# Kernel tuning notes

Measured on AMD Instinct MI355X. Metric: run time of the kernel, lower is better.

Reference implementation:

```python
import jax, jax.numpy as jnp
import numpy as np

N_P = 200000  # points (literals)
N_C = 50000   # constraints (clauses)
D = 64
VOCAB = 400   # max_size**2 = 20**2


def setup_inputs() -> dict:
    key = jax.random.key(0)
    ks = jax.random.split(key, 12)
    s = 0.05
    inp = {}
    inp["embedding"] = jax.random.normal(ks[0], (VOCAB, D)) * s
    inp["cls_bias"] = jnp.zeros((VOCAB,))
    inp["W_cinit"] = jax.random.normal(ks[1], (D, 1)) * s
    inp["b_cinit"] = jnp.zeros((D,))
    # clause LSTMs stacked in c_t order: 0=equi, 1=square, 2=diamond, 3=midpoint
    inp["Wih_c"] = jax.random.normal(ks[2], (4, 4 * D, 4 * D)) * s
    inp["Whh_c"] = jax.random.normal(ks[3], (4, 4 * D, D)) * s
    inp["bih_c"] = jnp.zeros((4, 4 * D))
    inp["bhh_c"] = jnp.zeros((4, 4 * D))
    # point-update LSTM L_u
    inp["Wih_u"] = jax.random.normal(ks[4], (4 * D, D)) * s
    inp["Whh_u"] = jax.random.normal(ks[5], (4 * D, D)) * s
    inp["bih_u"] = jnp.zeros((4 * D,))
    inp["bhh_u"] = jnp.zeros((4 * D,))
    inp["x_p_rand"] = jax.random.uniform(ks[6], (N_P, D))
    inp["y"] = jax.random.randint(ks[7], (N_P,), 0, VOCAB)
    inp["p_t"] = jax.random.randint(ks[8], (N_P,), 0, 2)
    inp["c_t"] = jax.random.randint(ks[9], (N_C,), 0, 4)
    inp["p2c"] = jax.random.randint(ks[10], (N_C, 4), 0, N_P)
    inp["num_iters"] = 2
    return inp


def _lstm_cell(x, h, c, Wih, Whh, bih, bhh):
    # torch nn.LSTM single-step cell, gate order (i, f, g, o)
    gates = x @ Wih.T + bih + h @ Whh.T + bhh
    i, f, g, o = jnp.split(gates, 4, axis=-1)
    c_new = jax.nn.sigmoid(f) * c + jax.nn.sigmoid(i) * jnp.tanh(g)
    h_new = jax.nn.sigmoid(o) * jnp.tanh(c_new)
    return h_new, c_new


def reference(embedding, cls_bias, W_cinit, b_cinit, Wih_c, Whh_c, bih_c, bhh_c,
              Wih_u, Whh_u, bih_u, bhh_u, x_p_rand, y, p_t, c_t, p2c, num_iters):
    n_p, d = x_p_rand.shape
    n_c = c_t.shape[0]
    fixed = (p_t != 0)[:, None]  # fixed points keep their embedding
    x_p = jnp.where(fixed, embedding[y], x_p_rand)
    c_init = W_cinit[:, 0] + b_cinit  # C_init(ones(1))
    x_c = jnp.broadcast_to(c_init, (n_c, d))
    x_p_h = jnp.zeros_like(x_p)
    x_c_h = jnp.zeros_like(x_c)
    sel = jax.nn.one_hot(c_t, 4, dtype=x_p.dtype)  # [n_c, 4] clause-type selector
    flat_p2c = p2c.reshape(-1)
    for _ in range(num_iters):
        # LC: gather the 4 points of each constraint
        vars_ = x_p[p2c]  # [n_c, 4, d]
        vars_full = vars_.reshape(n_c, 4 * d)
        vars_mid = vars_.at[:, 3].set(0.0).reshape(n_c, 4 * d)  # midpoint zeros 4th slot
        hs, cs = [], []
        for tp in range(4):
            inp_t = vars_mid if tp == 3 else vars_full
            h_t, c_new = _lstm_cell(inp_t, x_c, x_c_h, Wih_c[tp], Whh_c[tp], bih_c[tp], bhh_c[tp])
            hs.append(h_t)
            cs.append(c_new)
        hs = jnp.stack(hs)  # [4, n_c, d]
        cs = jnp.stack(cs)
        x_c = jnp.einsum('tnd,nt->nd', hs, sel)
        x_c_h = jnp.einsum('tnd,nt->nd', cs, sel)
        # CL: msg = adj.T @ x_c, i.e. scatter-add x_c over incidence edges
        msg = jax.ops.segment_sum(jnp.repeat(x_c, 4, axis=0), flat_p2c, num_segments=n_p)
        h_u, c_u = _lstm_cell(msg, x_p, x_p_h, Wih_u, Whh_u, bih_u, bhh_u)
        # only variable points are updated; fixed points keep old state
        x_p = jnp.where(fixed, x_p, h_u)
        x_p_h = jnp.where(fixed, x_p_h, c_u)
    logits = x_p @ embedding.T + cls_bias  # tied classifier
    return logits
```

## Files before the change

### kernel.cpp

```cpp
#include <hip/hip_runtime.h>
#include <hip/hip_bf16.h>

#define DD 64
#define GG 256

typedef __attribute__((ext_vector_type(8))) __bf16 bfrag;
typedef __attribute__((ext_vector_type(4))) float f32x4;

__device__ __forceinline__ float sigmf(float x){ return 1.f/(1.f+__expf(-x)); }
__device__ __forceinline__ float tanhfast(float x){ return 1.f - 2.f/(__expf(2.f*x)+1.f); }
__device__ __forceinline__ short bf16c(float f){
  __hip_bfloat16 h = __float2bfloat16(f);
  return *reinterpret_cast<short*>(&h);
}

__global__ void k_setup(
    const float* __restrict__ Wihc, const float* __restrict__ Whhc,
    const float* __restrict__ Wihu, const float* __restrict__ Whhu,
    const float* __restrict__ emb, const float* __restrict__ Wci,
    const float* __restrict__ bci, const float* __restrict__ xpr,
    const int* __restrict__ y, const int* __restrict__ pt,
    const int* __restrict__ ct, const int* __restrict__ p2c,
    short* __restrict__ Wc_lay, short* __restrict__ Wu_lay,
    short* __restrict__ E_lay,
    short* __restrict__ xp_bf, short* __restrict__ xc_bf,
    int* __restrict__ tlist, int* __restrict__ cnt,
    int* __restrict__ vlist, int* __restrict__ cnt2,
    int* __restrict__ deg, int NP, int NC)
{
  int b = blockIdx.x;
  const int t = threadIdx.x;
  if (b < 1280){
    int idx = b*256 + t;
    int tp = idx / 81920, r = idx % 81920;
    int ks = r / 8192;  int r2 = r % 8192;
    int nt = r2 / 512;  int r3 = r2 % 512;
    int lr = r3 / 32;   int r4 = r3 % 32;
    int lk = r4 / 8,    e  = r4 % 8;
    int g = nt*16 + lr, k = ks*32 + lk*8 + e;
    float v = (k < 256) ? Wihc[((size_t)tp*256+g)*256 + k]
                        : Whhc[((size_t)tp*256+g)*64 + (k-256)];
    Wc_lay[idx] = bf16c(v);
    return;
  }
  b -= 1280;
  if (b < 128){
    int idx = b*256 + t;
    int ks = idx / 8192; int r2 = idx % 8192;
    int nt = r2 / 512;   int r3 = r2 % 512;
    int lr = r3 / 32;    int r4 = r3 % 32;
    int lk = r4 / 8,     e  = r4 % 8;
    int g = nt*16 + lr, k = ks*32 + lk*8 + e;
    float v = (k < 64) ? Wihu[g*64 + k] : Whhu[g*64 + (k-64)];
    Wu_lay[idx] = bf16c(v);
    return;
  }
  b -= 128;
  if (b < 100){
    int idx = b*256 + t;
    int ks = idx / 12800; int r = idx % 12800;
    int nt = r / 512;     int r3 = r % 512;
    int lr = r3 / 32;     int r4 = r3 % 32;
    int lk = r4 / 8,      e  = r4 % 8;
    int v = nt*16 + lr, k = ks*32 + lk*8 + e;
    E_lay[idx] = bf16c(emb[v*64 + k]);
    return;
  }
  b -= 100;
  int nbP4 = (NP*4 + 255) >> 8;
  if (b < nbP4){
    int i = b*256 + t;
    if (i < NP*4){
      int p = i >> 2, ch = i & 3;
      const float* src = (pt[p]!=0) ? (emb + (size_t)y[p]*DD + ch*16)
                                    : (xpr + (size_t)p*DD + ch*16);
      short o[16];
      #pragma unroll
      for (int f4=0; f4<4; ++f4){
        float4 v = ((const float4*)src)[f4];
        o[f4*4+0]=bf16c(v.x); o[f4*4+1]=bf16c(v.y); o[f4*4+2]=bf16c(v.z); o[f4*4+3]=bf16c(v.w);
      }
      *(uint4*)(xp_bf + (size_t)p*DD + ch*16)     = *(uint4*)&o[0];
      *(uint4*)(xp_bf + (size_t)p*DD + ch*16 + 8) = *(uint4*)&o[8];
    }
    return;
  }
  b -= nbP4;
  int nbC4 = (NC*4 + 255) >> 8;
  if (b < nbC4){
    int i = b*256 + t;
    if (i < NC*4){
      int c = i >> 2, ch = i & 3;
      short o[16];
      #pragma unroll
      for (int d=0; d<16; ++d) o[d] = bf16c(Wci[ch*16+d] + bci[ch*16+d]);
      *(uint4*)(xc_bf + (size_t)c*DD + ch*16)     = *(uint4*)&o[0];
      *(uint4*)(xc_bf + (size_t)c*DD + ch*16 + 8) = *(uint4*)&o[8];
    }
    return;
  }
  b -= nbC4;
  int nbCl = (NC + 255) >> 8;
  if (b < nbCl){
    int c = b*256 + t;
    int lane = t & 63;
    int tp = (c < NC) ? ct[c] : -1;
    unsigned long long lt = (lane == 63) ? ~0ull >> 1 : ((1ull << lane) - 1ull);
    #pragma unroll
    for (int ty=0; ty<4; ++ty){
      unsigned long long m = __ballot(tp==ty);
      if (m == 0ull) continue;
      int nw = __popcll(m), rank = __popcll(m & lt);
      int leader = __ffsll((long long)m) - 1;
      int base = 0;
      if (lane == leader) base = atomicAdd(cnt + ty, nw);
      base = __shfl(base, leader);
      if (tp == ty) tlist[ty*NC + base + rank] = c;
    }
    return;
  }
  b -= nbCl;
  int nbCp = (NP + 255) >> 8;
  if (b < nbCp){
    int p = b*256 + t;
    int lane = t & 63;
    bool var = (p < NP) && (pt[p]==0);
    unsigned long long lt = (lane == 63) ? ~0ull >> 1 : ((1ull << lane) - 1ull);
    unsigned long long m = __ballot(var);
    if (m){
      int nw = __popcll(m), rank = __popcll(m & lt);
      int leader = __ffsll((long long)m) - 1;
      int base = 0;
      if (lane == leader) base = atomicAdd(cnt2, nw);
      base = __shfl(base, leader);
      if (var) vlist[base + rank] = p;
    }
    return;
  }
  b -= nbCp;
  {
    int e = b*256 + t;
    if (e < NC*4) atomicAdd(deg + p2c[e], 1);
  }
}

__global__ void k_rowstart(const int* __restrict__ deg, int* __restrict__ rowstart,
                           int* __restrict__ gtot, int NP){
  int p = blockIdx.x*256 + threadIdx.x;
  int lane = threadIdx.x & 63;
  int d = (p < NP) ? deg[p] : 0;
  int pre = d;
  #pragma unroll
  for (int off=1; off<64; off<<=1){
    int v = __shfl_up(pre, off);
    if (lane >= off) pre += v;
  }
  int tot = __shfl(pre, 63);
  int base = 0;
  if (lane == 63 && tot) base = atomicAdd(gtot, tot);
  base = __shfl(base, 63);
  if (p < NP) rowstart[p] = base + pre - d;
}
__global__ void k_fill(const int* __restrict__ p2c, const int* __restrict__ rowstart,
                       int* __restrict__ cursor, int* __restrict__ elist, int NE){
  int e = blockIdx.x*256 + threadIdx.x;
  if (e >= NE) return;
  int p = p2c[e];
  int pos = atomicAdd(cursor + p, 1);
  elist[rowstart[p] + pos] = e >> 2;
}

__launch_bounds__(256)
__global__ void k_clause(const short* __restrict__ Wc_lay,
                         const float* __restrict__ bih, const float* __restrict__ bhh,
                         const short* __restrict__ xp_bf,
                         short* __restrict__ xc_bf, float* __restrict__ xch,
                         const int* __restrict__ p2c, const int* __restrict__ tlist,
                         const int* __restrict__ cnt, int NC, int first){
  __shared__ __align__(16) short As[64][328];
  int tp, n, base;
  {
    const int c0=cnt[0], c1=cnt[1], c2=cnt[2], c3=cnt[3];
    int b = blockIdx.x;
    const int t0=(c0+63)>>6;
    if (b < t0){ tp=0; n=c0; base=b<<6; }
    else { b-=t0; const int t1=(c1+63)>>6;
      if (b < t1){ tp=1; n=c1; base=b<<6; }
      else { b-=t1; const int t2=(c2+63)>>6;
        if (b < t2){ tp=2; n=c2; base=b<<6; }
        else { b-=t2; const int t3=(c3+63)>>6;
          if (b < t3){ tp=3; n=c3; base=b<<6; } else return; } } }
  }
  const int t = threadIdx.x;
  {
    int row = t >> 2, ch = t & 3;
    int idx = base + row;
    int c = (idx < n) ? tlist[tp*NC + idx] : -1;
    #pragma unroll
    for (int slot=0; slot<5; ++slot){
      uint4 v0 = make_uint4(0,0,0,0), v1 = make_uint4(0,0,0,0);
      const short* src = nullptr;
      if (c >= 0){
        if (slot < 4){
          if (!(tp==3 && slot==3)){
            int p = p2c[c*4 + slot];
            src = xp_bf + (size_t)p*DD + ch*16;
          }
        } else src = xc_bf + (size_t)c*DD + ch*16;
      }
      if (src){ v0 = *(const uint4*)src; v1 = *(const uint4*)(src+8); }
      *(uint4*)&As[row][slot*64 + ch*16 + 0] = v0;
      *(uint4*)&As[row][slot*64 + ch*16 + 8] = v1;
    }
  }
  __syncthreads();
  const int lane = t & 63, w = t >> 6;
  const int lr = lane & 15, lk = lane >> 4;
  f32x4 acc[16];
  #pragma unroll
  for (int i=0;i<16;i++) acc[i] = (f32x4){0.f,0.f,0.f,0.f};
  const short* wb = Wc_lay + (size_t)tp*81920 + (lr*4 + lk)*8;
  #pragma unroll
  for (int ks=0; ks<10; ++ks){
    bfrag a = *(const bfrag*)&As[w*16 + lr][ks*32 + lk*8];
    #pragma unroll
    for (int nt=0; nt<16; ++nt){
      bfrag bv = *(const bfrag*)(wb + (ks*16 + nt)*512);
      acc[nt] = __builtin_amdgcn_mfma_f32_16x16x32_bf16(a, bv, acc[nt], 0, 0, 0);
    }
  }
  #pragma unroll
  for (int r=0; r<4; ++r){
    int idx = base + w*16 + lk*4 + r;
    if (idx >= n) continue;
    int c = tlist[tp*NC + idx];
    #pragma unroll
    for (int q=0; q<4; ++q){
      int d = lr + 16*q;
      float gi = acc[q][r]    + bih[tp*GG + d]       + bhh[tp*GG + d];
      float gf = acc[4+q][r]  + bih[tp*GG + 64 + d]  + bhh[tp*GG + 64 + d];
      float gn = acc[8+q][r]  + bih[tp*GG + 128 + d] + bhh[tp*GG + 128 + d];
      float go = acc[12+q][r] + bih[tp*GG + 192 + d] + bhh[tp*GG + 192 + d];
      float cold = first ? 0.f : xch[(size_t)c*DD + d];
      float cn = sigmf(gf)*cold + sigmf(gi)*tanhfast(gn);
      float hn = sigmf(go)*tanhfast(cn);
      xc_bf[(size_t)c*DD + d] = bf16c(hn);
      xch[(size_t)c*DD + d]   = cn;
    }
  }
}

__launch_bounds__(256)
__global__ void k_point(const short* __restrict__ Wu_lay,
                        const float* __restrict__ bihu, const float* __restrict__ bhhu,
                        const short* __restrict__ xc_bf,
                        const int* __restrict__ rowstart, const int* __restrict__ deg,
                        const int* __restrict__ elist, const int* __restrict__ vlist,
                        const int* __restrict__ nvp,
                        short* __restrict__ xp_bf, float* __restrict__ xph,
                        int NP, int first){
  const int nv = nvp[0];
  const int base = blockIdx.x*64;
  if (base >= nv) return;
  __shared__ __align__(16) short As[64][136];
  const int t = threadIdx.x;
  {
    int row = t >> 2, ch = t & 3;
    int idx = base + row;
    int gr = (idx < nv) ? vlist[idx] : -1;
    float s[16];
    #pragma unroll
    for (int z=0; z<16; ++z) s[z] = 0.f;
    uint4 xv0 = make_uint4(0,0,0,0), xv1 = make_uint4(0,0,0,0);
    if (gr >= 0){
      int rs = rowstart[gr], dg = deg[gr];
      for (int j=0; j<dg; ++j){
        int c = elist[rs + j];
        const uint4* xcp = (const uint4*)(xc_bf + (size_t)c*DD + ch*16);
        uint4 u0 = xcp[0], u1 = xcp[1];
        uint ua[8] = {u0.x,u0.y,u0.z,u0.w,u1.x,u1.y,u1.z,u1.w};
        #pragma unroll
        for (int i2=0;i2<8;i2++){
          s[i2*2]   += __uint_as_float(ua[i2] << 16);
          s[i2*2+1] += __uint_as_float(ua[i2] & 0xffff0000u);
        }
      }
      const uint4* xpp = (const uint4*)(xp_bf + (size_t)gr*DD + ch*16);
      xv0 = xpp[0]; xv1 = xpp[1];
    }
    short os[16];
    #pragma unroll
    for (int z=0; z<16; ++z) os[z] = bf16c(s[z]);
    *(uint4*)&As[row][ch*16 + 0] = *(uint4*)&os[0];
    *(uint4*)&As[row][ch*16 + 8] = *(uint4*)&os[8];
    *(uint4*)&As[row][64 + ch*16 + 0] = xv0;
    *(uint4*)&As[row][64 + ch*16 + 8] = xv1;
  }
  __syncthreads();
  const int lane = t & 63, w = t >> 6;
  const int lr = lane & 15, lk = lane >> 4;
  f32x4 acc[16];
  #pragma unroll
  for (int i=0;i<16;i++) acc[i] = (f32x4){0.f,0.f,0.f,0.f};
  const short* wb = Wu_lay + (lr*4 + lk)*8;
  #pragma unroll
  for (int ks=0; ks<4; ++ks){
    bfrag a = *(const bfrag*)&As[w*16 + lr][ks*32 + lk*8];
    #pragma unroll
    for (int nt=0; nt<16; ++nt){
      bfrag bv = *(const bfrag*)(wb + (ks*16 + nt)*512);
      acc[nt] = __builtin_amdgcn_mfma_f32_16x16x32_bf16(a, bv, acc[nt], 0, 0, 0);
    }
  }
  #pragma unroll
  for (int r=0; r<4; ++r){
    int idx = base + w*16 + lk*4 + r;
    if (idx >= nv) continue;
    int m = vlist[idx];
    #pragma unroll
    for (int q=0; q<4; ++q){
      int d = lr + 16*q;
      float gi = acc[q][r]    + bihu[d]       + bhhu[d];
      float gf = acc[4+q][r]  + bihu[64 + d]  + bhhu[64 + d];
      float gn = acc[8+q][r]  + bihu[128 + d] + bhhu[128 + d];
      float go = acc[12+q][r] + bihu[192 + d] + bhhu[192 + d];
      float cold = first ? 0.f : xph[(size_t)idx*DD + d];
      float cn = sigmf(gf)*cold + sigmf(gi)*tanhfast(gn);
      float hn = sigmf(go)*tanhfast(cn);
      xp_bf[(size_t)m*DD + d] = bf16c(hn);
      xph[(size_t)idx*DD + d] = cn;
    }
  }
}

__launch_bounds__(256)
__global__ void k_logits(const short* __restrict__ xp_bf, const short* __restrict__ E_lay,
                         const float* __restrict__ cbias,
                         float* __restrict__ out, int NP, int V){
  const int t = threadIdx.x;
  const int lane = t & 63, w = t >> 6;
  const int lr = lane & 15, lk = lane >> 4;
  const int p = blockIdx.x*64 + w*16 + lr;
  const int nt0 = blockIdx.y*5;
  const bool ok = p < NP;
  f32x4 acc[5];
  #pragma unroll
  for (int j=0;j<5;j++) acc[j] = (f32x4){0.f,0.f,0.f,0.f};
  const short* ab = E_lay + (lr*4 + lk)*8;
  #pragma unroll
  for (int ks=0; ks<2; ++ks){
    bfrag b;
    if (ok) b = *(const bfrag*)(xp_bf + (size_t)p*DD + ks*32 + lk*8);
    else    b = (bfrag){0,0,0,0,0,0,0,0};
    #pragma unroll
    for (int j=0; j<5; ++j){
      bfrag a = *(const bfrag*)(ab + (ks*25 + nt0 + j)*512);
      acc[j] = __builtin_amdgcn_mfma_f32_16x16x32_bf16(a, b, acc[j], 0, 0, 0);
    }
  }
  if (!ok) return;
  #pragma unroll
  for (int j=0; j<5; ++j){
    int v = (nt0 + j)*16 + lk*4;
    float4 cb = *(const float4*)(cbias + v);
    float4 r;
    r.x = acc[j][0] + cb.x;
    r.y = acc[j][1] + cb.y;
    r.z = acc[j][2] + cb.z;
    r.w = acc[j][3] + cb.w;
    *(float4*)(out + (size_t)p*V + v) = r;
  }
}

extern "C" void kernel_launch(void* const* d_in, const int* in_sizes, int n_in,
                              void* d_out, int out_size, void* d_ws, size_t ws_size,
                              hipStream_t stream){
  const float* emb   = (const float*)d_in[0];
  const float* cbias = (const float*)d_in[1];
  const float* Wci   = (const float*)d_in[2];
  const float* bci   = (const float*)d_in[3];
  const float* Wihc  = (const float*)d_in[4];
  const float* Whhc  = (const float*)d_in[5];
  const float* bihc  = (const float*)d_in[6];
  const float* bhhc  = (const float*)d_in[7];
  const float* Wihu  = (const float*)d_in[8];
  const float* Whhu  = (const float*)d_in[9];
  const float* bihu  = (const float*)d_in[10];
  const float* bhhu  = (const float*)d_in[11];
  const float* xpr   = (const float*)d_in[12];
  const int* y    = (const int*)d_in[13];
  const int* pt   = (const int*)d_in[14];
  const int* ct   = (const int*)d_in[15];
  const int* p2c  = (const int*)d_in[16];
  const int NP = in_sizes[13];
  const int NC = in_sizes[15];
  const int V  = in_sizes[1];
  const int NE = NC*4;

  char* w = (char*)d_ws;
  auto alloc = [&](size_t bytes)->char*{ char* p = w; w += (bytes + 255) & ~255ull; return p; };
  short* xp_bf = (short*)alloc((size_t)NP*DD*2);
  float* xph   = (float*)alloc((size_t)NP*DD*4);
  short* xc_bf = (short*)alloc((size_t)NC*DD*2);
  float* xch   = (float*)alloc((size_t)NC*DD*4);
  int*   tlist = (int*)alloc((size_t)4*NC*4);
  short* Wc_lay= (short*)alloc((size_t)327680*2);
  short* Wu_lay= (short*)alloc((size_t)32768*2);
  short* E_lay = (short*)alloc((size_t)25600*2);
  int*   deg     = (int*)alloc((size_t)NP*4);
  int*   cursor  = (int*)alloc((size_t)NP*4);
  int*   ctr     = (int*)alloc(256);
  int*   rowstart= (int*)alloc((size_t)NP*4);
  int*   elist   = (int*)alloc((size_t)NE*4);
  int*   vlist   = (int*)alloc((size_t)NP*4);
  int* cnt  = ctr;
  int* cnt2 = ctr + 16;
  int* gtot = ctr + 17;

  const int NB   = (NP + 255)/256;
  const int nbP4 = (NP*4 + 255)/256;
  const int nbC4 = (NC*4 + 255)/256;
  const int nbCl = (NC + 255)/256;
  const int nbCp = NB;
  const int nbE  = (NE + 255)/256;
  const int g_setup = 1280 + 128 + 100 + nbP4 + nbC4 + nbCl + nbCp + nbE;

  hipMemsetAsync(deg, 0, (size_t)NP*8 + 256, stream);
  k_setup<<<g_setup, 256, 0, stream>>>(Wihc, Whhc, Wihu, Whhu, emb, Wci, bci, xpr,
                                       y, pt, ct, p2c,
                                       Wc_lay, Wu_lay, E_lay,
                                       xp_bf, xc_bf,
                                       tlist, cnt, vlist, cnt2, deg, NP, NC);
  k_rowstart<<<NB, 256, 0, stream>>>(deg, rowstart, gtot, NP);
  k_fill<<<nbE, 256, 0, stream>>>(p2c, rowstart, cursor, elist, NE);

  const int ctiles = (NC+63)/64 + 3;
  const int num_iters = 2;
  for (int it=0; it<num_iters; ++it){
    k_clause<<<ctiles, 256, 0, stream>>>(Wc_lay, bihc, bhhc, xp_bf, xc_bf, xch,
                                         p2c, tlist, cnt, NC, it==0);
    k_point<<<(NP+63)/64, 256, 0, stream>>>(Wu_lay, bihu, bhhu, xc_bf,
                                            rowstart, deg, elist, vlist, cnt2,
                                            xp_bf, xph, NP, it==0);
  }
  const int ngv = (V/16 + 4)/5;
  k_logits<<<dim3((NP+63)/64, ngv), 256, 0, stream>>>(xp_bf, E_lay, cbias,
                                                      (float*)d_out, NP, V);
}
```

Before: 456.6 us.

## Fuse all stages into one persistent cooperative kernel with grid syncs

Replaces the memset, setup, rowstart, fill, per-iteration clause/point kernels and logits kernel with a single persistent cooperative kernel. Blocks loop over work items and separate stages with grid-wide syncs. The logits stage is also restructured so each block computes all vocab tiles per point tile in two accumulator batches. This removes multiple kernel launches and launch gaps. In exchange, grid.sync costs are added, occupancy is limited by launch_bounds(256,3) and the shared LDS buffer, and the grid is capped at 2048 blocks.

```diff
diff --git a/kernel.cpp b/kernel.cpp
--- a/kernel.cpp
+++ b/kernel.cpp
@@ -1,5 +1,8 @@
 #include <hip/hip_runtime.h>
 #include <hip/hip_bf16.h>
+#include <hip/hip_cooperative_groups.h>
+
+namespace cg = cooperative_groups;
 
 #define DD 64
 #define GG 256
@@ -14,361 +17,378 @@
   return *reinterpret_cast<short*>(&h);
 }
 
-__global__ void k_setup(
+__launch_bounds__(256, 3)
+__global__ void k_mega(
     const float* __restrict__ Wihc, const float* __restrict__ Whhc,
     const float* __restrict__ Wihu, const float* __restrict__ Whhu,
-    const float* __restrict__ emb, const float* __restrict__ Wci,
-    const float* __restrict__ bci, const float* __restrict__ xpr,
-    const int* __restrict__ y, const int* __restrict__ pt,
+    const float* __restrict__ emb,  const float* __restrict__ Wci,
+    const float* __restrict__ bci,  const float* __restrict__ xpr,
+    const int* __restrict__ y,  const int* __restrict__ pt,
     const int* __restrict__ ct, const int* __restrict__ p2c,
-    short* __restrict__ Wc_lay, short* __restrict__ Wu_lay,
-    short* __restrict__ E_lay,
-    short* __restrict__ xp_bf, short* __restrict__ xc_bf,
-    int* __restrict__ tlist, int* __restrict__ cnt,
-    int* __restrict__ vlist, int* __restrict__ cnt2,
-    int* __restrict__ deg, int NP, int NC)
+    const float* __restrict__ bihc, const float* __restrict__ bhhc,
+    const float* __restrict__ bihu, const float* __restrict__ bhhu,
+    const float* __restrict__ cbias,
+    short* __restrict__ Wc_lay, short* __restrict__ Wu_lay, short* __restrict__ E_lay,
+    short* __restrict__ xp_bf,  short* __restrict__ xc_bf,
+    float* __restrict__ xph,    float* __restrict__ xch,
+    int* __restrict__ tlist, int* __restrict__ vlist,
+    int* __restrict__ deg, int* __restrict__ cursor, int* __restrict__ ctr,
+    int* __restrict__ rowstart, int* __restrict__ elist,
+    float* __restrict__ out, int NP, int NC, int V)
 {
-  int b = blockIdx.x;
+  cg::grid_group grid = cg::this_grid();
+  __shared__ __align__(16) short As[64][328];
   const int t = threadIdx.x;
-  if (b < 1280){
-    int idx = b*256 + t;
-    int tp = idx / 81920, r = idx % 81920;
-    int ks = r / 8192;  int r2 = r % 8192;
-    int nt = r2 / 512;  int r3 = r2 % 512;
-    int lr = r3 / 32;   int r4 = r3 % 32;
-    int lk = r4 / 8,    e  = r4 % 8;
-    int g = nt*16 + lr, k = ks*32 + lk*8 + e;
-    float v = (k < 256) ? Wihc[((size_t)tp*256+g)*256 + k]
-                        : Whhc[((size_t)tp*256+g)*64 + (k-256)];
-    Wc_lay[idx] = bf16c(v);
-    return;
-  }
-  b -= 1280;
-  if (b < 128){
-    int idx = b*256 + t;
-    int ks = idx / 8192; int r2 = idx % 8192;
-    int nt = r2 / 512;   int r3 = r2 % 512;
-    int lr = r3 / 32;    int r4 = r3 % 32;
-    int lk = r4 / 8,     e  = r4 % 8;
-    int g = nt*16 + lr, k = ks*32 + lk*8 + e;
-    float v = (k < 64) ? Wihu[g*64 + k] : Whhu[g*64 + (k-64)];
-    Wu_lay[idx] = bf16c(v);
-    return;
-  }
-  b -= 128;
-  if (b < 100){
-    int idx = b*256 + t;
-    int ks = idx / 12800; int r = idx % 12800;
-    int nt = r / 512;     int r3 = r % 512;
-    int lr = r3 / 32;     int r4 = r3 % 32;
-    int lk = r4 / 8,      e  = r4 % 8;
-    int v = nt*16 + lr, k = ks*32 + lk*8 + e;
-    E_lay[idx] = bf16c(emb[v*64 + k]);
-    return;
-  }
-  b -= 100;
-  int nbP4 = (NP*4 + 255) >> 8;
-  if (b < nbP4){
-    int i = b*256 + t;
-    if (i < NP*4){
-      int p = i >> 2, ch = i & 3;
-      const float* src = (pt[p]!=0) ? (emb + (size_t)y[p]*DD + ch*16)
-                                    : (xpr + (size_t)p*DD + ch*16);
-      short o[16];
-      #pragma unroll
-      for (int f4=0; f4<4; ++f4){
-        float4 v = ((const float4*)src)[f4];
-        o[f4*4+0]=bf16c(v.x); o[f4*4+1]=bf16c(v.y); o[f4*4+2]=bf16c(v.z); o[f4*4+3]=bf16c(v.w);
-      }
-      *(uint4*)(xp_bf + (size_t)p*DD + ch*16)     = *(uint4*)&o[0];
-      *(uint4*)(xp_bf + (size_t)p*DD + ch*16 + 8) = *(uint4*)&o[8];
-    }
-    return;
-  }
-  b -= nbP4;
-  int nbC4 = (NC*4 + 255) >> 8;
-  if (b < nbC4){
-    int i = b*256 + t;
-    if (i < NC*4){
-      int c = i >> 2, ch = i & 3;
-      short o[16];
-      #pragma unroll
-      for (int d=0; d<16; ++d) o[d] = bf16c(Wci[ch*16+d] + bci[ch*16+d]);
-      *(uint4*)(xc_bf + (size_t)c*DD + ch*16)     = *(uint4*)&o[0];
-      *(uint4*)(xc_bf + (size_t)c*DD + ch*16 + 8) = *(uint4*)&o[8];
-    }
-    return;
-  }
-  b -= nbC4;
-  int nbCl = (NC + 255) >> 8;
-  if (b < nbCl){
-    int c = b*256 + t;
-    int lane = t & 63;
-    int tp = (c < NC) ? ct[c] : -1;
-    unsigned long long lt = (lane == 63) ? ~0ull >> 1 : ((1ull << lane) - 1ull);
-    #pragma unroll
-    for (int ty=0; ty<4; ++ty){
-      unsigned long long m = __ballot(tp==ty);
-      if (m == 0ull) continue;
-      int nw = __popcll(m), rank = __popcll(m & lt);
-      int leader = __ffsll((long long)m) - 1;
-      int base = 0;
-      if (lane == leader) base = atomicAdd(cnt + ty, nw);
-      base = __shfl(base, leader);
-      if (tp == ty) tlist[ty*NC + base + rank] = c;
-    }
-    return;
-  }
-  b -= nbCl;
-  int nbCp = (NP + 255) >> 8;
-  if (b < nbCp){
-    int p = b*256 + t;
-    int lane = t & 63;
-    bool var = (p < NP) && (pt[p]==0);
-    unsigned long long lt = (lane == 63) ? ~0ull >> 1 : ((1ull << lane) - 1ull);
-    unsigned long long m = __ballot(var);
-    if (m){
-      int nw = __popcll(m), rank = __popcll(m & lt);
-      int leader = __ffsll((long long)m) - 1;
-      int base = 0;
-      if (lane == leader) base = atomicAdd(cnt2, nw);
-      base = __shfl(base, leader);
-      if (var) vlist[base + rank] = p;
-    }
-    return;
-  }
-  b -= nbCp;
-  {
-    int e = b*256 + t;
-    if (e < NC*4) atomicAdd(deg + p2c[e], 1);
-  }
-}
-
-__global__ void k_rowstart(const int* __restrict__ deg, int* __restrict__ rowstart,
-                           int* __restrict__ gtot, int NP){
-  int p = blockIdx.x*256 + threadIdx.x;
-  int lane = threadIdx.x & 63;
-  int d = (p < NP) ? deg[p] : 0;
-  int pre = d;
-  #pragma unroll
-  for (int off=1; off<64; off<<=1){
-    int v = __shfl_up(pre, off);
-    if (lane >= off) pre += v;
-  }
-  int tot = __shfl(pre, 63);
-  int base = 0;
-  if (lane == 63 && tot) base = atomicAdd(gtot, tot);
-  base = __shfl(base, 63);
-  if (p < NP) rowstart[p] = base + pre - d;
-}
-__global__ void k_fill(const int* __restrict__ p2c, const int* __restrict__ rowstart,
-                       int* __restrict__ cursor, int* __restrict__ elist, int NE){
-  int e = blockIdx.x*256 + threadIdx.x;
-  if (e >= NE) return;
-  int p = p2c[e];
-  int pos = atomicAdd(cursor + p, 1);
-  elist[rowstart[p] + pos] = e >> 2;
-}
-
-__launch_bounds__(256)
-__global__ void k_clause(const short* __restrict__ Wc_lay,
-                         const float* __restrict__ bih, const float* __restrict__ bhh,
-                         const short* __restrict__ xp_bf,
-                         short* __restrict__ xc_bf, float* __restrict__ xch,
-                         const int* __restrict__ p2c, const int* __restrict__ tlist,
-                         const int* __restrict__ cnt, int NC, int first){
-  __shared__ __align__(16) short As[64][328];
-  int tp, n, base;
-  {
-    const int c0=cnt[0], c1=cnt[1], c2=cnt[2], c3=cnt[3];
-    int b = blockIdx.x;
-    const int t0=(c0+63)>>6;
-    if (b < t0){ tp=0; n=c0; base=b<<6; }
-    else { b-=t0; const int t1=(c1+63)>>6;
-      if (b < t1){ tp=1; n=c1; base=b<<6; }
-      else { b-=t1; const int t2=(c2+63)>>6;
-        if (b < t2){ tp=2; n=c2; base=b<<6; }
-        else { b-=t2; const int t3=(c3+63)>>6;
-          if (b < t3){ tp=3; n=c3; base=b<<6; } else return; } } }
-  }
-  const int t = threadIdx.x;
-  {
-    int row = t >> 2, ch = t & 3;
-    int idx = base + row;
-    int c = (idx < n) ? tlist[tp*NC + idx] : -1;
-    #pragma unroll
-    for (int slot=0; slot<5; ++slot){
-      uint4 v0 = make_uint4(0,0,0,0), v1 = make_uint4(0,0,0,0);
-      const short* src = nullptr;
-      if (c >= 0){
-        if (slot < 4){
-          if (!(tp==3 && slot==3)){
-            int p = p2c[c*4 + slot];
-            src = xp_bf + (size_t)p*DD + ch*16;
-          }
-        } else src = xc_bf + (size_t)c*DD + ch*16;
-      }
-      if (src){ v0 = *(const uint4*)src; v1 = *(const uint4*)(src+8); }
-      *(uint4*)&As[row][slot*64 + ch*16 + 0] = v0;
-      *(uint4*)&As[row][slot*64 + ch*16 + 8] = v1;
-    }
-  }
-  __syncthreads();
+  const int nblk = gridDim.x;
   const int lane = t & 63, w = t >> 6;
   const int lr = lane & 15, lk = lane >> 4;
-  f32x4 acc[16];
-  #pragma unroll
-  for (int i=0;i<16;i++) acc[i] = (f32x4){0.f,0.f,0.f,0.f};
-  const short* wb = Wc_lay + (size_t)tp*81920 + (lr*4 + lk)*8;
-  #pragma unroll
-  for (int ks=0; ks<10; ++ks){
-    bfrag a = *(const bfrag*)&As[w*16 + lr][ks*32 + lk*8];
-    #pragma unroll
-    for (int nt=0; nt<16; ++nt){
-      bfrag bv = *(const bfrag*)(wb + (ks*16 + nt)*512);
-      acc[nt] = __builtin_amdgcn_mfma_f32_16x16x32_bf16(a, bv, acc[nt], 0, 0, 0);
+  int* cnt  = ctr;
+  int* cnt2 = ctr + 16;
+  int* gtot = ctr + 17;
+  const int NE = NC*4;
+
+  for (int i = blockIdx.x*256 + t; i < NP; i += nblk*256) deg[i] = 0;
+  for (int i = blockIdx.x*256 + t; i < NP; i += nblk*256) cursor[i] = 0;
+  if (blockIdx.x == 0 && t < 64) ctr[t] = 0;
+  grid.sync();
+
+  {
+    const int nbP4 = (NP*4 + 255) >> 8;
+    const int nbC4 = (NC*4 + 255) >> 8;
+    const int nbCl = (NC + 255) >> 8;
+    const int nbCp = (NP + 255) >> 8;
+    const int nbE  = (NE + 255) >> 8;
+    const int W = 1280 + 128 + 100 + nbP4 + nbC4 + nbCl + nbCp + nbE;
+    for (int wk = blockIdx.x; wk < W; wk += nblk){
+      int b = wk;
+      if (b < 1280){
+        int idx = b*256 + t;
+        int tp = idx / 81920, r = idx % 81920;
+        int ks = r / 8192;  int r2 = r % 8192;
+        int nt = r2 / 512;  int r3 = r2 % 512;
+        int lrr = r3 / 32;  int r4 = r3 % 32;
+        int lkk = r4 / 8,   e  = r4 % 8;
+        int g = nt*16 + lrr, k = ks*32 + lkk*8 + e;
+        float v = (k < 256) ? Wihc[((size_t)tp*256+g)*256 + k]
+                            : Whhc[((size_t)tp*256+g)*64 + (k-256)];
+        Wc_lay[idx] = bf16c(v);
+      } else if ((b -= 1280) < 128){
+        int idx = b*256 + t;
+        int ks = idx / 8192; int r2 = idx % 8192;
+        int nt = r2 / 512;   int r3 = r2 % 512;
+        int lrr = r3 / 32;   int r4 = r3 % 32;
+        int lkk = r4 / 8,    e  = r4 % 8;
+        int g = nt*16 + lrr, k = ks*32 + lkk*8 + e;
+        float v = (k < 64) ? Wihu[g*64 + k] : Whhu[g*64 + (k-64)];
+        Wu_lay[idx] = bf16c(v);
+      } else if ((b -= 128) < 100){
+        int idx = b*256 + t;
+        int ks = idx / 12800; int r = idx % 12800;
+        int nt = r / 512;     int r3 = r % 512;
+        int lrr = r3 / 32;    int r4 = r3 % 32;
+        int lkk = r4 / 8,     e  = r4 % 8;
+        int v = nt*16 + lrr, k = ks*32 + lkk*8 + e;
+        E_lay[idx] = bf16c(emb[v*64 + k]);
+      } else if ((b -= 100) < nbP4){
+        int i = b*256 + t;
+        if (i < NP*4){
+          int p = i >> 2, ch = i & 3;
+          const float* src = (pt[p]!=0) ? (emb + (size_t)y[p]*DD + ch*16)
+                                        : (xpr + (size_t)p*DD + ch*16);
+          short o[16];
+          #pragma unroll
+          for (int f4=0; f4<4; ++f4){
+            float4 v = ((const float4*)src)[f4];
+            o[f4*4+0]=bf16c(v.x); o[f4*4+1]=bf16c(v.y); o[f4*4+2]=bf16c(v.z); o[f4*4+3]=bf16c(v.w);
+          }
+          *(uint4*)(xp_bf + (size_t)p*DD + ch*16)     = *(uint4*)&o[0];
+          *(uint4*)(xp_bf + (size_t)p*DD + ch*16 + 8) = *(uint4*)&o[8];
+        }
+      } else if ((b -= nbP4) < nbC4){
+        int i = b*256 + t;
+        if (i < NC*4){
+          int c = i >> 2, ch = i & 3;
+          short o[16];
+          #pragma unroll
+          for (int d=0; d<16; ++d) o[d] = bf16c(Wci[ch*16+d] + bci[ch*16+d]);
+          *(uint4*)(xc_bf + (size_t)c*DD + ch*16)     = *(uint4*)&o[0];
+          *(uint4*)(xc_bf + (size_t)c*DD + ch*16 + 8) = *(uint4*)&o[8];
+        }
+      } else if ((b -= nbC4) < nbCl){
+        int c = b*256 + t;
+        int tp = (c < NC) ? ct[c] : -1;
+        unsigned long long lt = (lane == 63) ? ~0ull >> 1 : ((1ull << lane) - 1ull);
+        #pragma unroll
+        for (int ty=0; ty<4; ++ty){
+          unsigned long long m = __ballot(tp==ty);
+          if (m == 0ull) continue;
+          int nw = __popcll(m), rank = __popcll(m & lt);
+          int leader = __ffsll((long long)m) - 1;
+          int base = 0;
+          if (lane == leader) base = atomicAdd(cnt + ty, nw);
+          base = __shfl(base, leader);
+          if (tp == ty) tlist[ty*NC + base + rank] = c;
+        }
+      } else if ((b -= nbCl) < nbCp){
+        int p = b*256 + t;
+        bool var = (p < NP) && (pt[p]==0);
+        unsigned long long lt = (lane == 63) ? ~0ull >> 1 : ((1ull << lane) - 1ull);
+        unsigned long long m = __ballot(var);
+        if (m){
+          int nw = __popcll(m), rank = __popcll(m & lt);
+          int leader = __ffsll((long long)m) - 1;
+          int base = 0;
+          if (lane == leader) base = atomicAdd(cnt2, nw);
+          base = __shfl(base, leader);
+          if (var) vlist[base + rank] = p;
+        }
+      } else {
+        b -= nbCp;
+        int e = b*256 + t;
+        if (e < NE) atomicAdd(deg + p2c[e], 1);
+      }
     }
   }
-  #pragma unroll
-  for (int r=0; r<4; ++r){
-    int idx = base + w*16 + lk*4 + r;
-    if (idx >= n) continue;
-    int c = tlist[tp*NC + idx];
-    #pragma unroll
-    for (int q=0; q<4; ++q){
-      int d = lr + 16*q;
-      float gi = acc[q][r]    + bih[tp*GG + d]       + bhh[tp*GG + d];
-      float gf = acc[4+q][r]  + bih[tp*GG + 64 + d]  + bhh[tp*GG + 64 + d];
-      float gn = acc[8+q][r]  + bih[tp*GG + 128 + d] + bhh[tp*GG + 128 + d];
-      float go = acc[12+q][r] + bih[tp*GG + 192 + d] + bhh[tp*GG + 192 + d];
-      float cold = first ? 0.f : xch[(size_t)c*DD + d];
-      float cn = sigmf(gf)*cold + sigmf(gi)*tanhfast(gn);
-      float hn = sigmf(go)*tanhfast(cn);
-      xc_bf[(size_t)c*DD + d] = bf16c(hn);
-      xch[(size_t)c*DD + d]   = cn;
+  grid.sync();
+
+  {
+    const int NB = (NP + 255) >> 8;
+    for (int tb = blockIdx.x; tb < NB; tb += nblk){
+      int p = tb*256 + t;
+      int d = (p < NP) ? deg[p] : 0;
+      int pre = d;
+      #pragma unroll
+      for (int off=1; off<64; off<<=1){
+        int v = __shfl_up(pre, off);
+        if (lane >= off) pre += v;
+      }
+      int tot = __shfl(pre, 63);
+      int base = 0;
+      if (lane == 63 && tot) base = atomicAdd(gtot, tot);
+      base = __shfl(base, 63);
+      if (p < NP) rowstart[p] = base + pre - d;
     }
   }
-}
-
-__launch_bounds__(256)
-__global__ void k_point(const short* __restrict__ Wu_lay,
-                        const float* __restrict__ bihu, const float* __restrict__ bhhu,
-                        const short* __restrict__ xc_bf,
-                        const int* __restrict__ rowstart, const int* __restrict__ deg,
-                        const int* __restrict__ elist, const int* __restrict__ vlist,
-                        const int* __restrict__ nvp,
-                        short* __restrict__ xp_bf, float* __restrict__ xph,
-                        int NP, int first){
-  const int nv = nvp[0];
-  const int base = blockIdx.x*64;
-  if (base >= nv) return;
-  __shared__ __align__(16) short As[64][136];
-  const int t = threadIdx.x;
+  grid.sync();
+
   {
-    int row = t >> 2, ch = t & 3;
-    int idx = base + row;
-    int gr = (idx < nv) ? vlist[idx] : -1;
-    float s[16];
-    #pragma unroll
-    for (int z=0; z<16; ++z) s[z] = 0.f;
-    uint4 xv0 = make_uint4(0,0,0,0), xv1 = make_uint4(0,0,0,0);
-    if (gr >= 0){
-      int rs = rowstart[gr], dg = deg[gr];
-      for (int j=0; j<dg; ++j){
-        int c = elist[rs + j];
-        const uint4* xcp = (const uint4*)(xc_bf + (size_t)c*DD + ch*16);
-        uint4 u0 = xcp[0], u1 = xcp[1];
-        uint ua[8] = {u0.x,u0.y,u0.z,u0.w,u1.x,u1.y,u1.z,u1.w};
-        #pragma unroll
-        for (int i2=0;i2<8;i2++){
-          s[i2*2]   += __uint_as_float(ua[i2] << 16);
-          s[i2*2+1] += __uint_as_float(ua[i2] & 0xffff0000u);
-        }
-      }
-      const uint4* xpp = (const uint4*)(xp_bf + (size_t)gr*DD + ch*16);
-      xv0 = xpp[0]; xv1 = xpp[1];
-    }
-    short os[16];
-    #pragma unroll
-    for (int z=0; z<16; ++z) os[z] = bf16c(s[z]);
-    *(uint4*)&As[row][ch*16 + 0] = *(uint4*)&os[0];
-    *(uint4*)&As[row][ch*16 + 8] = *(uint4*)&os[8];
-    *(uint4*)&As[row][64 + ch*16 + 0] = xv0;
-    *(uint4*)&As[row][64 + ch*16 + 8] = xv1;
+    const int nbE = (NE + 255) >> 8;
+    for (int tb = blockIdx.x; tb < nbE; tb += nblk){
+      int e = tb*256 + t;
+      if (e < NE){
+        int p = p2c[e];
+        int pos = atomicAdd(cursor + p, 1);
+        elist[rowstart[p] + pos] = e >> 2;
+      }
+    }
   }
-  __syncthreads();
-  const int lane = t & 63, w = t >> 6;
-  const int lr = lane & 15, lk = lane >> 4;
-  f32x4 acc[16];
-  #pragma unroll
-  for (int i=0;i<16;i++) acc[i] = (f32x4){0.f,0.f,0.f,0.f};
-  const short* wb = Wu_lay + (lr*4 + lk)*8;
-  #pragma unroll
-  for (int ks=0; ks<4; ++ks){
-    bfrag a = *(const bfrag*)&As[w*16 + lr][ks*32 + lk*8];
-    #pragma unroll
-    for (int nt=0; nt<16; ++nt){
-      bfrag bv = *(const bfrag*)(wb + (ks*16 + nt)*512);
-      acc[nt] = __builtin_amdgcn_mfma_f32_16x16x32_bf16(a, bv, acc[nt], 0, 0, 0);
-    }
+  grid.sync();
+
+  for (int it=0; it<2; ++it){
+    const int first = (it==0);
+    {
+      const int c0=cnt[0], c1=cnt[1], c2=cnt[2], c3=cnt[3];
+      const int t0=(c0+63)>>6, t1=(c1+63)>>6, t2=(c2+63)>>6, t3=(c3+63)>>6;
+      const int ctiles = t0+t1+t2+t3;
+      for (int tile = blockIdx.x; tile < ctiles; tile += nblk){
+        int b = tile, tp, n, base;
+        if (b < t0){ tp=0; n=c0; base=b<<6; }
+        else { b-=t0; if (b < t1){ tp=1; n=c1; base=b<<6; }
+          else { b-=t1; if (b < t2){ tp=2; n=c2; base=b<<6; }
+            else { b-=t2; tp=3; n=c3; base=b<<6; } } }
+        __syncthreads();
+        {
+          int row = t >> 2, ch = t & 3;
+          int idx = base + row;
+          int c = (idx < n) ? tlist[tp*NC + idx] : -1;
+          #pragma unroll
+          for (int slot=0; slot<5; ++slot){
+            uint4 v0 = make_uint4(0,0,0,0), v1 = make_uint4(0,0,0,0);
+            const short* src = nullptr;
+            if (c >= 0){
+              if (slot < 4){
+                if (!(tp==3 && slot==3)){
+                  int p = p2c[c*4 + slot];
+                  src = xp_bf + (size_t)p*DD + ch*16;
+                }
+              } else src = xc_bf + (size_t)c*DD + ch*16;
+            }
+            if (src){ v0 = *(const uint4*)src; v1 = *(const uint4*)(src+8); }
+            *(uint4*)&As[row][slot*64 + ch*16 + 0] = v0;
+            *(uint4*)&As[row][slot*64 + ch*16 + 8] = v1;
+          }
+        }
+        __syncthreads();
+        f32x4 acc[16];
+        #pragma unroll
+        for (int i=0;i<16;i++) acc[i] = (f32x4){0.f,0.f,0.f,0.f};
+        const short* wb = Wc_lay + (size_t)tp*81920 + (lr*4 + lk)*8;
+        #pragma unroll
+        for (int ks=0; ks<10; ++ks){
+          bfrag a = *(const bfrag*)&As[w*16 + lr][ks*32 + lk*8];
+          #pragma unroll
+          for (int nt=0; nt<16; ++nt){
+            bfrag bv = *(const bfrag*)(wb + (ks*16 + nt)*512);
+            acc[nt] = __builtin_amdgcn_mfma_f32_16x16x32_bf16(a, bv, acc[nt], 0, 0, 0);
+          }
+        }
+        #pragma unroll
+        for (int r=0; r<4; ++r){
+          int idx = base + w*16 + lk*4 + r;
+          if (idx >= n) continue;
+          int c = tlist[tp*NC + idx];
+          #pragma unroll
+          for (int q=0; q<4; ++q){
+            int d = lr + 16*q;
+            float gi = acc[q][r]    + bihc[tp*GG + d]       + bhhc[tp*GG + d];
+            float gf = acc[4+q][r]  + bihc[tp*GG + 64 + d]  + bhhc[tp*GG + 64 + d];
+            float gn = acc[8+q][r]  + bihc[tp*GG + 128 + d] + bhhc[tp*GG + 128 + d];
+            float go = acc[12+q][r] + bihc[tp*GG + 192 + d] + bhhc[tp*GG + 192 + d];
+            float cold = first ? 0.f : xch[(size_t)c*DD + d];
+            float cn = sigmf(gf)*cold + sigmf(gi)*tanhfast(gn);
+            float hn = sigmf(go)*tanhfast(cn);
+            xc_bf[(size_t)c*DD + d] = bf16c(hn);
+            xch[(size_t)c*DD + d]   = cn;
+          }
+        }
+      }
+    }
+    grid.sync();
+    {
+      const int nv = cnt2[0];
+      const int ptiles = (nv + 63) >> 6;
+      short (*Ap)[136] = (short (*)[136])&As[0][0];
+      for (int tile = blockIdx.x; tile < ptiles; tile += nblk){
+        const int base = tile*64;
+        __syncthreads();
+        {
+          int row = t >> 2, ch = t & 3;
+          int idx = base + row;
+          int gr = (idx < nv) ? vlist[idx] : -1;
+          float s[16];
+          #pragma unroll
+          for (int z=0; z<16; ++z) s[z] = 0.f;
+          uint4 xv0 = make_uint4(0,0,0,0), xv1 = make_uint4(0,0,0,0);
+          if (gr >= 0){
+            int rs = rowstart[gr], dg = deg[gr];
+            for (int j=0; j<dg; ++j){
+              int c = elist[rs + j];
+              const uint4* xcp = (const uint4*)(xc_bf + (size_t)c*DD + ch*16);
+              uint4 u0 = xcp[0], u1 = xcp[1];
+              uint ua[8] = {u0.x,u0.y,u0.z,u0.w,u1.x,u1.y,u1.z,u1.w};
+              #pragma unroll
+              for (int i2=0;i2<8;i2++){
+                s[i2*2]   += __uint_as_float(ua[i2] << 16);
+                s[i2*2+1] += __uint_as_float(ua[i2] & 0xffff0000u);
+              }
+            }
+            const uint4* xpp = (const uint4*)(xp_bf + (size_t)gr*DD + ch*16);
+            xv0 = xpp[0]; xv1 = xpp[1];
+          }
+          short os[16];
+          #pragma unroll
+          for (int z=0; z<16; ++z) os[z] = bf16c(s[z]);
+          *(uint4*)&Ap[row][ch*16 + 0] = *(uint4*)&os[0];
+          *(uint4*)&Ap[row][ch*16 + 8] = *(uint4*)&os[8];
+          *(uint4*)&Ap[row][64 + ch*16 + 0] = xv0;
+          *(uint4*)&Ap[row][64 + ch*16 + 8] = xv1;
+        }
+        __syncthreads();
+        f32x4 acc[16];
+        #pragma unroll
+        for (int i=0;i<16;i++) acc[i] = (f32x4){0.f,0.f,0.f,0.f};
+        const short* wb = Wu_lay + (lr*4 + lk)*8;
+        #pragma unroll
+        for (int ks=0; ks<4; ++ks){
+          bfrag a = *(const bfrag*)&Ap[w*16 + lr][ks*32 + lk*8];
+          #pragma unroll
+          for (int nt=0; nt<16; ++nt){
+            bfrag bv = *(const bfrag*)(wb + (ks*16 + nt)*512);
+            acc[nt] = __builtin_amdgcn_mfma_f32_16x16x32_bf16(a, bv, acc[nt], 0, 0, 0);
+          }
+        }
+        #pragma unroll
+        for (int r=0; r<4; ++r){
+          int idx = base + w*16 + lk*4 + r;
+          if (idx >= nv) continue;
+          int m = vlist[idx];
+          #pragma unroll
+          for (int q=0; q<4; ++q){
+            int d = lr + 16*q;
+            float gi = acc[q][r]    + bihu[d]       + bhhu[d];
+            float gf = acc[4+q][r]  + bihu[64 + d]  + bhhu[64 + d];
+            float gn = acc[8+q][r]  + bihu[128 + d] + bhhu[128 + d];
+            float go = acc[12+q][r] + bihu[192 + d] + bhhu[192 + d];
+            float cold = first ? 0.f : xph[(size_t)idx*DD + d];
+            float cn = sigmf(gf)*cold + sigmf(gi)*tanhfast(gn);
+            float hn = sigmf(go)*tanhfast(cn);
+            xp_bf[(size_t)m*DD + d] = bf16c(hn);
+            xph[(size_t)idx*DD + d] = cn;
+          }
+        }
+      }
+    }
+    grid.sync();
   }
-  #pragma unroll
-  for (int r=0; r<4; ++r){
-    int idx = base + w*16 + lk*4 + r;
-    if (idx >= nv) continue;
-    int m = vlist[idx];
-    #pragma unroll
-    for (int q=0; q<4; ++q){
-      int d = lr + 16*q;
-      float gi = acc[q][r]    + bihu[d]       + bhhu[d];
-      float gf = acc[4+q][r]  + bihu[64 + d]  + bhhu[64 + d];
-      float gn = acc[8+q][r]  + bihu[128 + d] + bhhu[128 + d];
-      float go = acc[12+q][r] + bihu[192 + d] + bhhu[192 + d];
-      float cold = first ? 0.f : xph[(size_t)idx*DD + d];
-      float cn = sigmf(gf)*cold + sigmf(gi)*tanhfast(gn);
-      float hn = sigmf(go)*tanhfast(cn);
-      xp_bf[(size_t)m*DD + d] = bf16c(hn);
-      xph[(size_t)idx*DD + d] = cn;
-    }
-  }
-}
-
-__launch_bounds__(256)
-__global__ void k_logits(const short* __restrict__ xp_bf, const short* __restrict__ E_lay,
-                         const float* __restrict__ cbias,
-                         float* __restrict__ out, int NP, int V){
-  const int t = threadIdx.x;
-  const int lane = t & 63, w = t >> 6;
-  const int lr = lane & 15, lk = lane >> 4;
-  const int p = blockIdx.x*64 + w*16 + lr;
-  const int nt0 = blockIdx.y*5;
-  const bool ok = p < NP;
-  f32x4 acc[5];
-  #pragma unroll
-  for (int j=0;j<5;j++) acc[j] = (f32x4){0.f,0.f,0.f,0.f};
-  const short* ab = E_lay + (lr*4 + lk)*8;
-  #pragma unroll
-  for (int ks=0; ks<2; ++ks){
-    bfrag b;
-    if (ok) b = *(const bfrag*)(xp_bf + (size_t)p*DD + ks*32 + lk*8);
-    else    b = (bfrag){0,0,0,0,0,0,0,0};
-    #pragma unroll
-    for (int j=0; j<5; ++j){
-      bfrag a = *(const bfrag*)(ab + (ks*25 + nt0 + j)*512);
-      acc[j] = __builtin_amdgcn_mfma_f32_16x16x32_bf16(a, b, acc[j], 0, 0, 0);
-    }
-  }
-  if (!ok) return;
-  #pragma unroll
-  for (int j=0; j<5; ++j){
-    int v = (nt0 + j)*16 + lk*4;
-    float4 cb = *(const float4*)(cbias + v);
-    float4 r;
-    r.x = acc[j][0] + cb.x;
-    r.y = acc[j][1] + cb.y;
-    r.z = acc[j][2] + cb.z;
-    r.w = acc[j][3] + cb.w;
-    *(float4*)(out + (size_t)p*V + v) = r;
+
+  {
+    const int ltiles = (NP + 63) >> 6;
+    for (int tile = blockIdx.x; tile < ltiles; tile += nblk){
+      int p = tile*64 + w*16 + lr;
+      bool ok = p < NP;
+      bfrag b0, b1;
+      if (ok){
+        b0 = *(const bfrag*)(xp_bf + (size_t)p*DD + lk*8);
+        b1 = *(const bfrag*)(xp_bf + (size_t)p*DD + 32 + lk*8);
+      } else { b0 = (bfrag){0,0,0,0,0,0,0,0}; b1 = b0; }
+      const short* ab = E_lay + (lr*4 + lk)*8;
+      {
+        f32x4 acc[13];
+        #pragma unroll
+        for (int j=0;j<13;j++) acc[j] = (f32x4){0.f,0.f,0.f,0.f};
+        #pragma unroll
+        for (int j=0;j<13;j++){
+          bfrag a0 = *(const bfrag*)(ab + j*512);
+          acc[j] = __builtin_amdgcn_mfma_f32_16x16x32_bf16(a0, b0, acc[j], 0, 0, 0);
+          bfrag a1 = *(const bfrag*)(ab + (25 + j)*512);
+          acc[j] = __builtin_amdgcn_mfma_f32_16x16x32_bf16(a1, b1, acc[j], 0, 0, 0);
+        }
+        if (ok){
+          #pragma unroll
+          for (int j=0;j<13;j++){
+            int v = j*16 + lk*4;
+            float4 cb = *(const float4*)(cbias + v);
+            float4 r;
+            r.x = acc[j][0] + cb.x; r.y = acc[j][1] + cb.y;
+            r.z = acc[j][2] + cb.z; r.w = acc[j][3] + cb.w;
+            *(float4*)(out + (size_t)p*V + v) = r;
+          }
+        }
+      }
+      {
+        f32x4 acc[12];
+        #pragma unroll
+        for (int j=0;j<12;j++) acc[j] = (f32x4){0.f,0.f,0.f,0.f};
+        #pragma unroll
+        for (int j=0;j<12;j++){
+          bfrag a0 = *(const bfrag*)(ab + (13 + j)*512);
+          acc[j] = __builtin_amdgcn_mfma_f32_16x16x32_bf16(a0, b0, acc[j], 0, 0, 0);
+          bfrag a1 = *(const bfrag*)(ab + (25 + 13 + j)*512);
+          acc[j] = __builtin_amdgcn_mfma_f32_16x16x32_bf16(a1, b1, acc[j], 0, 0, 0);
+        }
+        if (ok){
+          #pragma unroll
+          for (int j=0;j<12;j++){
+            int v = (13 + j)*16 + lk*4;
+            float4 cb = *(const float4*)(cbias + v);
+            float4 r;
+            r.x = acc[j][0] + cb.x; r.y = acc[j][1] + cb.y;
+            r.z = acc[j][2] + cb.z; r.w = acc[j][3] + cb.w;
+            *(float4*)(out + (size_t)p*V + v) = r;
+          }
+        }
+      }
+    }
   }
 }
 
@@ -392,13 +412,13 @@
   const int* pt   = (const int*)d_in[14];
   const int* ct   = (const int*)d_in[15];
   const int* p2c  = (const int*)d_in[16];
-  const int NP = in_sizes[13];
-  const int NC = in_sizes[15];
-  const int V  = in_sizes[1];
+  int NP = in_sizes[13];
+  int NC = in_sizes[15];
+  int V  = in_sizes[1];
   const int NE = NC*4;
 
-  char* w = (char*)d_ws;
-  auto alloc = [&](size_t bytes)->char*{ char* p = w; w += (bytes + 255) & ~255ull; return p; };
+  char* wsp = (char*)d_ws;
+  auto alloc = [&](size_t bytes)->char*{ char* p = wsp; wsp += (bytes + 255) & ~255ull; return p; };
   short* xp_bf = (short*)alloc((size_t)NP*DD*2);
   float* xph   = (float*)alloc((size_t)NP*DD*4);
   short* xc_bf = (short*)alloc((size_t)NC*DD*2);
@@ -413,37 +433,25 @@
   int*   rowstart= (int*)alloc((size_t)NP*4);
   int*   elist   = (int*)alloc((size_t)NE*4);
   int*   vlist   = (int*)alloc((size_t)NP*4);
-  int* cnt  = ctr;
-  int* cnt2 = ctr + 16;
-  int* gtot = ctr + 17;
-
-  const int NB   = (NP + 255)/256;
-  const int nbP4 = (NP*4 + 255)/256;
-  const int nbC4 = (NC*4 + 255)/256;
-  const int nbCl = (NC + 255)/256;
-  const int nbCp = NB;
-  const int nbE  = (NE + 255)/256;
-  const int g_setup = 1280 + 128 + 100 + nbP4 + nbC4 + nbCl + nbCp + nbE;
-
-  hipMemsetAsync(deg, 0, (size_t)NP*8 + 256, stream);
-  k_setup<<<g_setup, 256, 0, stream>>>(Wihc, Whhc, Wihu, Whhu, emb, Wci, bci, xpr,
-                                       y, pt, ct, p2c,
-                                       Wc_lay, Wu_lay, E_lay,
-                                       xp_bf, xc_bf,
-                                       tlist, cnt, vlist, cnt2, deg, NP, NC);
-  k_rowstart<<<NB, 256, 0, stream>>>(deg, rowstart, gtot, NP);
-  k_fill<<<nbE, 256, 0, stream>>>(p2c, rowstart, cursor, elist, NE);
-
-  const int ctiles = (NC+63)/64 + 3;
-  const int num_iters = 2;
-  for (int it=0; it<num_iters; ++it){
-    k_clause<<<ctiles, 256, 0, stream>>>(Wc_lay, bihc, bhhc, xp_bf, xc_bf, xch,
-                                         p2c, tlist, cnt, NC, it==0);
-    k_point<<<(NP+63)/64, 256, 0, stream>>>(Wu_lay, bihu, bhhu, xc_bf,
-                                            rowstart, deg, elist, vlist, cnt2,
-                                            xp_bf, xph, NP, it==0);
-  }
-  const int ngv = (V/16 + 4)/5;
-  k_logits<<<dim3((NP+63)/64, ngv), 256, 0, stream>>>(xp_bf, E_lay, cbias,
-                                                      (float*)d_out, NP, V);
+  float* out = (float*)d_out;
+
+  int maxb = 0;
+  hipOccupancyMaxActiveBlocksPerMultiprocessor(&maxb, (const void*)k_mega, 256, 0);
+  if (maxb < 1) maxb = 1;
+  int grid = maxb * 256;
+  if (grid > 2048) grid = 2048;
+
+  void* args[] = {
+    (void*)&Wihc, (void*)&Whhc, (void*)&Wihu, (void*)&Whhu,
+    (void*)&emb,  (void*)&Wci,  (void*)&bci,  (void*)&xpr,
+    (void*)&y, (void*)&pt, (void*)&ct, (void*)&p2c,
+    (void*)&bihc, (void*)&bhhc, (void*)&bihu, (void*)&bhhu,
+    (void*)&cbias,
+    (void*)&Wc_lay, (void*)&Wu_lay, (void*)&E_lay,
+    (void*)&xp_bf, (void*)&xc_bf, (void*)&xph, (void*)&xch,
+    (void*)&tlist, (void*)&vlist, (void*)&deg, (void*)&cursor, (void*)&ctr,
+    (void*)&rowstart, (void*)&elist,
+    (void*)&out, (void*)&NP, (void*)&NC, (void*)&V
+  };
+  hipLaunchCooperativeKernel((const void*)k_mega, dim3(grid), dim3(256), args, 0, stream);
 }
```

After: 1.129 ms. 147% more time.
